# Kernel optimization log

Measured on AMD Instinct MI355X. Metric: run time of the kernel, lower is better.

The kernel has to match this reference:

```python
import jax, jax.numpy as jnp
import numpy as np

N_NODES = 50000
N_EDGES = 800000
IN_DIM = 128
HID_DIM = 128
OUT_DIM = 128
NEG_SLOPE = 0.2


def setup_inputs() -> dict:
    key = jax.random.key(0)
    ks = jax.random.split(key, 12)
    x = jax.random.normal(ks[0], (N_NODES, IN_DIM), dtype=jnp.float32)
    edge_index = jax.random.randint(ks[1], (2, N_EDGES), 0, N_NODES, dtype=jnp.int64)
    edge_weight = jax.random.uniform(ks[2], (N_EDGES,), dtype=jnp.float32)
    # Glorot-ish init for weights, zeros for bias (PyG GATConv defaults)
    s1 = 1.0 / np.sqrt(IN_DIM)
    s2 = 1.0 / np.sqrt(HID_DIM)
    W1 = jax.random.normal(ks[3], (IN_DIM, HID_DIM), dtype=jnp.float32) * s1
    a_src1 = jax.random.normal(ks[4], (HID_DIM,), dtype=jnp.float32) * s2
    a_dst1 = jax.random.normal(ks[5], (HID_DIM,), dtype=jnp.float32) * s2
    b1 = jnp.zeros((HID_DIM,), dtype=jnp.float32)
    W2 = jax.random.normal(ks[6], (HID_DIM, OUT_DIM), dtype=jnp.float32) * s2
    a_src2 = jax.random.normal(ks[7], (OUT_DIM,), dtype=jnp.float32) * (1.0 / np.sqrt(OUT_DIM))
    a_dst2 = jax.random.normal(ks[8], (OUT_DIM,), dtype=jnp.float32) * (1.0 / np.sqrt(OUT_DIM))
    b2 = jnp.zeros((OUT_DIM,), dtype=jnp.float32)
    return {"x": x, "edge_index": edge_index, "edge_weight": edge_weight,
            "W1": W1, "a_src1": a_src1, "a_dst1": a_dst1, "b1": b1,
            "W2": W2, "a_src2": a_src2, "a_dst2": a_dst2, "b2": b2}


def _gat_layer(x, src, dst, W, a_src, a_dst, b, n_nodes):
    # Linear transform: [N, F_out]
    h = x @ W
    # Per-node attention logits (heads=1): scalar per node
    al_src = h @ a_src  # [N]
    al_dst = h @ a_dst  # [N]
    # Edge-wise raw attention, LeakyReLU(negative_slope=0.2)
    e = al_src[src] + al_dst[dst]                     # [E]
    e = jnp.where(e >= 0, e, NEG_SLOPE * e)
    # Numerically stable segment softmax over incoming edges of dst
    m = jax.ops.segment_max(e, dst, num_segments=n_nodes)   # [N]
    ex = jnp.exp(e - m[dst])                                # [E]
    denom = jax.ops.segment_sum(ex, dst, num_segments=n_nodes)  # [N]
    alpha = ex / denom[dst]                                 # [E]
    # Attention-weighted scatter-add aggregation
    out = jax.ops.segment_sum(alpha[:, None] * h[src], dst, num_segments=n_nodes)
    return out + b


def reference(x, edge_index, edge_weight, W1, a_src1, a_dst1, b1, W2, a_src2, a_dst2, b2):
    n = x.shape[0]
    # PyG GATConv default add_self_loops=True; edge_weight (edge_attr) is
    # ignored because edge_dim=None in GATConv(in, out, heads=1).
    loop = jnp.arange(n, dtype=edge_index.dtype)
    src = jnp.concatenate([edge_index[0], loop])
    dst = jnp.concatenate([edge_index[1], loop])
    h = jax.nn.relu(_gat_layer(x, src, dst, W1, a_src1, a_dst1, b1, n))
    out = jax.nn.relu(_gat_layer(h, src, dst, W2, a_src2, a_dst2, b2, n))
    return out
```

## Files before the change

kernel.cpp:

```cpp
#include <hip/hip_runtime.h>
#include <hip/hip_bf16.h>
#include <hip/hip_fp16.h>
#include <type_traits>

#define DIM 128
#define NEG_SLOPE 0.2f
#define LDSP 136
#define CAP 64
#define NB 256
#define SUBCAP 32

typedef _Float16 half8 __attribute__((ext_vector_type(8)));
typedef float floatx4 __attribute__((ext_vector_type(4)));

__device__ __forceinline__ void bucket_body(int bb, const int* __restrict__ src,
                                            const int* __restrict__ dst,
                                            int* __restrict__ bcnt,
                                            int2* __restrict__ arena,
                                            int E, int npb, int nblk,
                                            int* lhist) {
    int tid = threadIdx.x;
    if (tid < NB) lhist[tid] = 0;
    __syncthreads();

    int base = bb * 2048;
    int dd[8], ss[8], rk[8], bk[8];
#pragma unroll
    for (int k = 0; k < 8; ++k) {
        int i = base + k * 256 + tid;
        if (i < E) {
            dd[k] = dst[i];
            ss[k] = src[i];
            bk[k] = dd[k] / npb;
            rk[k] = atomicAdd(&lhist[bk[k]], 1);
        } else {
            bk[k] = -1;
        }
    }
    __syncthreads();

    if (tid < NB) {
        int c = lhist[tid];
        bcnt[(size_t)tid * nblk + bb] = (c < SUBCAP) ? c : SUBCAP;
    }

#pragma unroll
    for (int k = 0; k < 8; ++k) {
        if (bk[k] >= 0 && rk[k] < SUBCAP) {
            arena[((size_t)bk[k] * nblk + bb) * SUBCAP + rk[k]] = make_int2(dd[k], ss[k]);
        }
    }
}

template <typename TIN>
__device__ __forceinline__ void gemm_body(int gb, const TIN* __restrict__ X,
                                          const float* __restrict__ W,
                                          __half* __restrict__ Hh,
                                          const float* __restrict__ a_src,
                                          const float* __restrict__ a_dst,
                                          float* __restrict__ alsrc,
                                          float* __restrict__ aldst, int n,
                                          _Float16* Ws) {
    int tid = threadIdx.x;
    int row0 = gb * 64;

    for (int e = tid; e < DIM * DIM; e += 256) {
        int k = e >> 7, c = e & 127;
        Ws[c * LDSP + k] = (_Float16)W[e];
    }

    int lane = tid & 63;
    int w = tid >> 6;
    int lo = lane & 15, hi = lane >> 4;

    int arow = row0 + w * 16 + lo;
    int ar = (arow < n) ? arow : (n - 1);
    half8 av[4];
#pragma unroll
    for (int t = 0; t < 4; ++t) {
        if constexpr (std::is_same<TIN, float>::value) {
            float4 v0 = *(const float4*)&X[(size_t)ar * DIM + t * 32 + hi * 8];
            float4 v1 = *(const float4*)&X[(size_t)ar * DIM + t * 32 + hi * 8 + 4];
            half8 h = {(_Float16)v0.x, (_Float16)v0.y, (_Float16)v0.z, (_Float16)v0.w,
                       (_Float16)v1.x, (_Float16)v1.y, (_Float16)v1.z, (_Float16)v1.w};
            av[t] = h;
        } else {
            av[t] = *(const half8*)&X[(size_t)ar * DIM + t * 32 + hi * 8];
        }
    }
    __syncthreads();

    floatx4 acc[8] = {};
#pragma unroll
    for (int t = 0; t < 4; ++t) {
#pragma unroll
        for (int f = 0; f < 8; ++f) {
            half8 bv = *(half8*)&Ws[(f * 16 + lo) * LDSP + t * 32 + hi * 8];
            acc[f] = __builtin_amdgcn_mfma_f32_16x16x32_f16(av[t], bv, acc[f], 0, 0, 0);
        }
    }

    float als[8], ald[8];
#pragma unroll
    for (int f = 0; f < 8; ++f) {
        als[f] = a_src[f * 16 + lo];
        ald[f] = a_dst[f * 16 + lo];
    }
#pragma unroll
    for (int r = 0; r < 4; ++r) {
        int grow = row0 + w * 16 + hi * 4 + r;
        float ps = 0.f, pd = 0.f;
#pragma unroll
        for (int f = 0; f < 8; ++f) {
            float v = acc[f][r];
            ps = fmaf(v, als[f], ps);
            pd = fmaf(v, ald[f], pd);
        }
#pragma unroll
        for (int o = 1; o <= 8; o <<= 1) {
            ps += __shfl_xor(ps, o);
            pd += __shfl_xor(pd, o);
        }
        if (grow < n) {
#pragma unroll
            for (int f = 0; f < 8; ++f)
                Hh[(size_t)grow * DIM + f * 16 + lo] = __float2half(acc[f][r]);
            if (lo == 0) { alsrc[grow] = ps; aldst[grow] = pd; }
        }
    }
}

__global__ __launch_bounds__(256, 4) void fused_bucket_gemm1(
        const int* __restrict__ esrc, const int* __restrict__ edst,
        int* __restrict__ bcnt, int2* __restrict__ arena, int E, int npb,
        int nBucket,
        const float* __restrict__ X, const float* __restrict__ W1,
        __half* __restrict__ Hh, const float* __restrict__ a_src,
        const float* __restrict__ a_dst, float* __restrict__ alsrc,
        float* __restrict__ aldst, int n) {
    __shared__ _Float16 Ws[DIM * LDSP];
    __shared__ int lhist[NB];
    int b = blockIdx.x;
    if (b < nBucket)
        bucket_body(b, esrc, edst, bcnt, arena, E, npb, nBucket, lhist);
    else
        gemm_body<float>(b - nBucket, X, W1, Hh, a_src, a_dst, alsrc, aldst, n, Ws);
}

__global__ __launch_bounds__(256, 4) void gemm2_kernel(const _Float16* __restrict__ X,
                                                       const float* __restrict__ W2,
                                                       __half* __restrict__ Hh,
                                                       const float* __restrict__ a_src,
                                                       const float* __restrict__ a_dst,
                                                       float* __restrict__ alsrc,
                                                       float* __restrict__ aldst, int n) {
    __shared__ _Float16 Ws[DIM * LDSP];
    gemm_body<_Float16>(blockIdx.x, X, W2, Hh, a_src, a_dst, alsrc, aldst, n, Ws);
}

__global__ __launch_bounds__(512) void build_kernel(const int2* __restrict__ arena,
                                                    const int* __restrict__ bcnt,
                                                    int* __restrict__ cnt,
                                                    int* __restrict__ csr,
                                                    int n, int npb, int nblk) {
    __shared__ int lcnt[NB];
    int B = blockIdx.x;
    int tid = threadIdx.x;
    int dlo = B * npb;

    if (tid < npb) lcnt[tid] = 0;
    __syncthreads();

    for (int c = tid; c < nblk; c += 512) {
        int m = bcnt[(size_t)B * nblk + c];
        const int2* ap = &arena[((size_t)B * nblk + c) * SUBCAP];
        for (int i = 0; i < m; ++i) {
            int2 e = ap[i];
            int li = e.x - dlo;
            if (li >= 0 && li < npb) {
                int r = atomicAdd(&lcnt[li], 1);
                if (r < CAP) csr[(size_t)e.x * CAP + r] = e.y;
            }
        }
    }
    __syncthreads();

    if (tid < npb) {
        int d = dlo + tid;
        if (d < n) {
            int c = lcnt[tid];
            cnt[d] = (c < CAP) ? c : CAP;
        }
    }
}

template <bool OUT16>
__global__ __launch_bounds__(256) void agg_kernel(const __half* __restrict__ Hh,
                                                  const int* __restrict__ cnt,
                                                  const int* __restrict__ csr,
                                                  const float* __restrict__ alsrc,
                                                  const float* __restrict__ aldst,
                                                  const float* __restrict__ bias,
                                                  void* __restrict__ OUTp, int n) {
    int wid = (blockIdx.x * 256 + threadIdx.x) >> 6;
    int lane = threadIdx.x & 63;
    if (wid >= n) return;

    int deg = cnt[wid];
    deg = (deg < CAP) ? deg : CAP;
    float ald = aldst[wid];

    float e_self = alsrc[wid] + ald;
    e_self = (e_self >= 0.f) ? e_self : NEG_SLOPE * e_self;

    int sIdx = 0;
    float eL = -INFINITY;
    if (lane < deg) {
        sIdx = csr[(size_t)wid * CAP + lane];
        float e = alsrc[sIdx] + ald;
        eL = (e >= 0.f) ? e : NEG_SLOPE * e;
    }
    float m = fmaxf(e_self, eL);
#pragma unroll
    for (int o = 32; o > 0; o >>= 1) m = fmaxf(m, __shfl_xor(m, o));

    float wL = (lane < deg) ? __expf(eL - m) : 0.f;
    float dsum = wL;
#pragma unroll
    for (int o = 32; o > 0; o >>= 1) dsum += __shfl_xor(dsum, o);

    float wS = __expf(e_self - m);
    float denom = wS + dsum;

    int half = lane >> 5;
    int fl = (lane & 31) * 4;
    float a0 = 0.f, a1 = 0.f, a2 = 0.f, a3 = 0.f;
    int degP = (deg + 15) & ~15;

    for (int j = 0; j < degP; j += 16) {
        int s[8]; float w[8]; uint2 h[8];
#pragma unroll
        for (int q = 0; q < 8; ++q) {
            int idx = j + 2 * q + half;
            s[q] = __shfl(sIdx, idx);
            w[q] = __shfl(wL, idx);
        }
#pragma unroll
        for (int q = 0; q < 8; ++q)
            h[q] = *(const uint2*)&Hh[(size_t)s[q] * DIM + fl];
#pragma unroll
        for (int q = 0; q < 8; ++q) {
            float2 fa = __half22float2(*(__half2*)&h[q].x);
            float2 fb = __half22float2(*(__half2*)&h[q].y);
            a0 = fmaf(w[q], fa.x, a0);
            a1 = fmaf(w[q], fa.y, a1);
            a2 = fmaf(w[q], fb.x, a2);
            a3 = fmaf(w[q], fb.y, a3);
        }
    }

    a0 += __shfl_xor(a0, 32);
    a1 += __shfl_xor(a1, 32);
    a2 += __shfl_xor(a2, 32);
    a3 += __shfl_xor(a3, 32);

    if (half == 0) {
        uint2 hs = *(const uint2*)&Hh[(size_t)wid * DIM + fl];
        float2 ha = __half22float2(*(__half2*)&hs.x);
        float2 hb = __half22float2(*(__half2*)&hs.y);
        a0 = fmaf(wS, ha.x, a0);
        a1 = fmaf(wS, ha.y, a1);
        a2 = fmaf(wS, hb.x, a2);
        a3 = fmaf(wS, hb.y, a3);

        float inv = 1.0f / denom;
        float4 bv = *(const float4*)&bias[fl];
        float o0 = fmaxf(fmaf(a0, inv, bv.x), 0.0f);
        float o1 = fmaxf(fmaf(a1, inv, bv.y), 0.0f);
        float o2 = fmaxf(fmaf(a2, inv, bv.z), 0.0f);
        float o3 = fmaxf(fmaf(a3, inv, bv.w), 0.0f);
        if constexpr (OUT16) {
            __half2 p0 = __floats2half2_rn(o0, o1);
            __half2 p1 = __floats2half2_rn(o2, o3);
            uint2 u;
            u.x = *(unsigned int*)&p0;
            u.y = *(unsigned int*)&p1;
            *(uint2*)&((__half*)OUTp)[(size_t)wid * DIM + fl] = u;
        } else {
            *(float4*)&((float*)OUTp)[(size_t)wid * DIM + fl] = make_float4(o0, o1, o2, o3);
        }
    }
}

extern "C" void kernel_launch(void* const* d_in, const int* in_sizes, int n_in,
                              void* d_out, int out_size, void* d_ws, size_t ws_size,
                              hipStream_t stream) {
    const float* x      = (const float*)d_in[0];
    const int*   eidx   = (const int*)d_in[1];
    const float* W1     = (const float*)d_in[3];
    const float* asrc1  = (const float*)d_in[4];
    const float* adst1  = (const float*)d_in[5];
    const float* b1     = (const float*)d_in[6];
    const float* W2     = (const float*)d_in[7];
    const float* asrc2  = (const float*)d_in[8];
    const float* adst2  = (const float*)d_in[9];
    const float* b2     = (const float*)d_in[10];
    float* out = (float*)d_out;

    int n = in_sizes[0] / DIM;
    int E = in_sizes[1] / 2;
    const int* esrc = eidx;
    const int* edst = eidx + E;

    int npb = (n + NB - 1) / NB;
    int nBucket = (E + 2047) / 2048;

    __half* Hh     = (__half*)d_ws;
    __half* y1h    = Hh + (size_t)n * DIM;
    float* alsrc   = (float*)(y1h + (size_t)n * DIM);
    float* aldst   = alsrc + n;
    int*   cnt     = (int*)(aldst + n);
    int*   csr     = cnt + n;
    int*   bcnt    = csr + (size_t)n * CAP;
    int2*  arena   = (int2*)(bcnt + (size_t)NB * nBucket);

    int gemm_grid = (n + 63) / 64;
    int wave_grid = (n + 3) / 4;

    fused_bucket_gemm1<<<nBucket + gemm_grid, 256, 0, stream>>>(
        esrc, edst, bcnt, arena, E, npb, nBucket,
        x, W1, Hh, asrc1, adst1, alsrc, aldst, n);

    build_kernel<<<NB, 512, 0, stream>>>(arena, bcnt, cnt, csr, n, npb, nBucket);

    agg_kernel<true><<<wave_grid, 256, 0, stream>>>(Hh, cnt, csr, alsrc, aldst, b1, y1h, n);

    gemm2_kernel<<<gemm_grid, 256, 0, stream>>>((const _Float16*)y1h, W2, Hh, asrc2, adst2, alsrc, aldst, n);
    agg_kernel<false><<<wave_grid, 256, 0, stream>>>(Hh, cnt, csr, alsrc, aldst, b2, out, n);
}
```

Before: 123.8 us.

## Fuse layer-2 linear transform and attention logits into layer-1 aggregation kernel

The separate gemm2 kernel is removed. The layer-1 aggregation kernel now stages W2 as fp16 in LDS per block, writes each node's ReLU output into a small LDS row, and computes that node's layer-2 features and attention logits with a per-wave mat-vec. This saves the y1h write and re-read plus one kernel launch. In exchange, every 8-node block reloads and converts the full W2 matrix, the mat-vec uses scalar FMAs instead of matrix instructions, and the larger LDS footprint may lower occupancy.

```diff
diff --git a/kernel.cpp b/kernel.cpp
--- a/kernel.cpp
+++ b/kernel.cpp
@@ -147,17 +147,6 @@
         gemm_body<float>(b - nBucket, X, W1, Hh, a_src, a_dst, alsrc, aldst, n, Ws);
 }
 
-__global__ __launch_bounds__(256, 4) void gemm2_kernel(const _Float16* __restrict__ X,
-                                                       const float* __restrict__ W2,
-                                                       __half* __restrict__ Hh,
-                                                       const float* __restrict__ a_src,
-                                                       const float* __restrict__ a_dst,
-                                                       float* __restrict__ alsrc,
-                                                       float* __restrict__ aldst, int n) {
-    __shared__ _Float16 Ws[DIM * LDSP];
-    gemm_body<_Float16>(blockIdx.x, X, W2, Hh, a_src, a_dst, alsrc, aldst, n, Ws);
-}
-
 __global__ __launch_bounds__(512) void build_kernel(const int2* __restrict__ arena,
                                                     const int* __restrict__ bcnt,
                                                     int* __restrict__ cnt,
@@ -194,16 +183,28 @@
     }
 }
 
-template <bool OUT16>
-__global__ __launch_bounds__(256) void agg_kernel(const __half* __restrict__ Hh,
-                                                  const int* __restrict__ cnt,
-                                                  const int* __restrict__ csr,
-                                                  const float* __restrict__ alsrc,
-                                                  const float* __restrict__ aldst,
-                                                  const float* __restrict__ bias,
-                                                  void* __restrict__ OUTp, int n) {
-    int wid = (blockIdx.x * 256 + threadIdx.x) >> 6;
-    int lane = threadIdx.x & 63;
+__global__ __launch_bounds__(512) void agg1_fused_kernel(
+        const __half* __restrict__ Hh, const int* __restrict__ cnt,
+        const int* __restrict__ csr, const float* __restrict__ alsrc,
+        const float* __restrict__ aldst, const float* __restrict__ bias1,
+        const float* __restrict__ W2, const float* __restrict__ asrc2,
+        const float* __restrict__ adst2,
+        __half* __restrict__ H2h, float* __restrict__ alsrc2,
+        float* __restrict__ aldst2, int n) {
+    __shared__ unsigned int w2p[DIM * 64];
+    __shared__ float yb[8][DIM];
+
+    int tid = threadIdx.x;
+    for (int e = tid * 2; e < DIM * DIM; e += 512 * 2) {
+        float2 v = *(const float2*)&W2[e];
+        __half2 h = __floats2half2_rn(v.x, v.y);
+        w2p[e >> 1] = *(unsigned int*)&h;
+    }
+    __syncthreads();
+
+    int wv = tid >> 6;
+    int lane = tid & 63;
+    int wid = blockIdx.x * 8 + wv;
     if (wid >= n) return;
 
     int deg = cnt[wid];
@@ -274,21 +275,126 @@
         a3 = fmaf(wS, hb.y, a3);
 
         float inv = 1.0f / denom;
+        float4 bv = *(const float4*)&bias1[fl];
+        float y0 = fmaxf(fmaf(a0, inv, bv.x), 0.0f);
+        float y1v = fmaxf(fmaf(a1, inv, bv.y), 0.0f);
+        float y2 = fmaxf(fmaf(a2, inv, bv.z), 0.0f);
+        float y3 = fmaxf(fmaf(a3, inv, bv.w), 0.0f);
+        *(float4*)&yb[wv][fl] = make_float4(y0, y1v, y2, y3);
+    }
+    asm volatile("s_waitcnt lgkmcnt(0)" ::: "memory");
+
+    float h2a = 0.f, h2b = 0.f;
+    for (int k4 = 0; k4 < 32; ++k4) {
+        float ya[4];
+        *(float4*)ya = *(float4*)&yb[wv][k4 * 4];
+#pragma unroll
+        for (int j = 0; j < 4; ++j) {
+            unsigned int wp = w2p[(k4 * 4 + j) * 64 + lane];
+            float2 wf = __half22float2(*(__half2*)&wp);
+            h2a = fmaf(ya[j], wf.x, h2a);
+            h2b = fmaf(ya[j], wf.y, h2b);
+        }
+    }
+
+    float ps = h2a * asrc2[2 * lane] + h2b * asrc2[2 * lane + 1];
+    float pd = h2a * adst2[2 * lane] + h2b * adst2[2 * lane + 1];
+#pragma unroll
+    for (int o = 1; o <= 32; o <<= 1) {
+        ps += __shfl_xor(ps, o);
+        pd += __shfl_xor(pd, o);
+    }
+    if (lane == 0) { alsrc2[wid] = ps; aldst2[wid] = pd; }
+
+    __half2 hh = __floats2half2_rn(h2a, h2b);
+    *(__half2*)&H2h[(size_t)wid * DIM + lane * 2] = hh;
+}
+
+__global__ __launch_bounds__(256) void agg2_kernel(const __half* __restrict__ Hh,
+                                                   const int* __restrict__ cnt,
+                                                   const int* __restrict__ csr,
+                                                   const float* __restrict__ alsrc,
+                                                   const float* __restrict__ aldst,
+                                                   const float* __restrict__ bias,
+                                                   float* __restrict__ OUT, int n) {
+    int wid = (blockIdx.x * 256 + threadIdx.x) >> 6;
+    int lane = threadIdx.x & 63;
+    if (wid >= n) return;
+
+    int deg = cnt[wid];
+    deg = (deg < CAP) ? deg : CAP;
+    float ald = aldst[wid];
+
+    float e_self = alsrc[wid] + ald;
+    e_self = (e_self >= 0.f) ? e_self : NEG_SLOPE * e_self;
+
+    int sIdx = 0;
+    float eL = -INFINITY;
+    if (lane < deg) {
+        sIdx = csr[(size_t)wid * CAP + lane];
+        float e = alsrc[sIdx] + ald;
+        eL = (e >= 0.f) ? e : NEG_SLOPE * e;
+    }
+    float m = fmaxf(e_self, eL);
+#pragma unroll
+    for (int o = 32; o > 0; o >>= 1) m = fmaxf(m, __shfl_xor(m, o));
+
+    float wL = (lane < deg) ? __expf(eL - m) : 0.f;
+    float dsum = wL;
+#pragma unroll
+    for (int o = 32; o > 0; o >>= 1) dsum += __shfl_xor(dsum, o);
+
+    float wS = __expf(e_self - m);
+    float denom = wS + dsum;
+
+    int half = lane >> 5;
+    int fl = (lane & 31) * 4;
+    float a0 = 0.f, a1 = 0.f, a2 = 0.f, a3 = 0.f;
+    int degP = (deg + 15) & ~15;
+
+    for (int j = 0; j < degP; j += 16) {
+        int s[8]; float w[8]; uint2 h[8];
+#pragma unroll
+        for (int q = 0; q < 8; ++q) {
+            int idx = j + 2 * q + half;
+            s[q] = __shfl(sIdx, idx);
+            w[q] = __shfl(wL, idx);
+        }
+#pragma unroll
+        for (int q = 0; q < 8; ++q)
+            h[q] = *(const uint2*)&Hh[(size_t)s[q] * DIM + fl];
+#pragma unroll
+        for (int q = 0; q < 8; ++q) {
+            float2 fa = __half22float2(*(__half2*)&h[q].x);
+            float2 fb = __half22float2(*(__half2*)&h[q].y);
+            a0 = fmaf(w[q], fa.x, a0);
+            a1 = fmaf(w[q], fa.y, a1);
+            a2 = fmaf(w[q], fb.x, a2);
+            a3 = fmaf(w[q], fb.y, a3);
+        }
+    }
+
+    a0 += __shfl_xor(a0, 32);
+    a1 += __shfl_xor(a1, 32);
+    a2 += __shfl_xor(a2, 32);
+    a3 += __shfl_xor(a3, 32);
+
+    if (half == 0) {
+        uint2 hs = *(const uint2*)&Hh[(size_t)wid * DIM + fl];
+        float2 ha = __half22float2(*(__half2*)&hs.x);
+        float2 hb = __half22float2(*(__half2*)&hs.y);
+        a0 = fmaf(wS, ha.x, a0);
+        a1 = fmaf(wS, ha.y, a1);
+        a2 = fmaf(wS, hb.x, a2);
+        a3 = fmaf(wS, hb.y, a3);
+
+        float inv = 1.0f / denom;
         float4 bv = *(const float4*)&bias[fl];
         float o0 = fmaxf(fmaf(a0, inv, bv.x), 0.0f);
         float o1 = fmaxf(fmaf(a1, inv, bv.y), 0.0f);
         float o2 = fmaxf(fmaf(a2, inv, bv.z), 0.0f);
         float o3 = fmaxf(fmaf(a3, inv, bv.w), 0.0f);
-        if constexpr (OUT16) {
-            __half2 p0 = __floats2half2_rn(o0, o1);
-            __half2 p1 = __floats2half2_rn(o2, o3);
-            uint2 u;
-            u.x = *(unsigned int*)&p0;
-            u.y = *(unsigned int*)&p1;
-            *(uint2*)&((__half*)OUTp)[(size_t)wid * DIM + fl] = u;
-        } else {
-            *(float4*)&((float*)OUTp)[(size_t)wid * DIM + fl] = make_float4(o0, o1, o2, o3);
-        }
+        *(float4*)&OUT[(size_t)wid * DIM + fl] = make_float4(o0, o1, o2, o3);
     }
 }
 
@@ -316,10 +422,12 @@
     int nBucket = (E + 2047) / 2048;
 
     __half* Hh     = (__half*)d_ws;
-    __half* y1h    = Hh + (size_t)n * DIM;
-    float* alsrc   = (float*)(y1h + (size_t)n * DIM);
+    __half* H2h    = Hh + (size_t)n * DIM;
+    float* alsrc   = (float*)(H2h + (size_t)n * DIM);
     float* aldst   = alsrc + n;
-    int*   cnt     = (int*)(aldst + n);
+    float* alsrc2  = aldst + n;
+    float* aldst2  = alsrc2 + n;
+    int*   cnt     = (int*)(aldst2 + n);
     int*   csr     = cnt + n;
     int*   bcnt    = csr + (size_t)n * CAP;
     int2*  arena   = (int2*)(bcnt + (size_t)NB * nBucket);
@@ -333,8 +441,9 @@
 
     build_kernel<<<NB, 512, 0, stream>>>(arena, bcnt, cnt, csr, n, npb, nBucket);
 
-    agg_kernel<true><<<wave_grid, 256, 0, stream>>>(Hh, cnt, csr, alsrc, aldst, b1, y1h, n);
-
-    gemm2_kernel<<<gemm_grid, 256, 0, stream>>>((const _Float16*)y1h, W2, Hh, asrc2, adst2, alsrc, aldst, n);
-    agg_kernel<false><<<wave_grid, 256, 0, stream>>>(Hh, cnt, csr, alsrc, aldst, b2, out, n);
-}
+    agg1_fused_kernel<<<(n + 7) / 8, 512, 0, stream>>>(
+        Hh, cnt, csr, alsrc, aldst, b1, W2, asrc2, adst2,
+        H2h, alsrc2, aldst2, n);
+
+    agg2_kernel<<<wave_grid, 256, 0, stream>>>(H2h, cnt, csr, alsrc2, aldst2, b2, out, n);
+}
```

Result: slower. 165.4 us (+33.7%).
